# Performance work log

Measured on AMD Instinct MI355X. Metric: run time of the kernel, lower is better.

The kernel has to match this reference:

```python
import jax, jax.numpy as jnp
import numpy as np

T, B, I, H, O = 512, 128, 256, 1024, 256


def setup_inputs() -> dict:
    key = jax.random.key(0)
    ks = jax.random.split(key, 16)
    std = 0.02
    inp = {
        "input_seq": jax.random.normal(ks[0], (T, B, I), dtype=jnp.float32),
        # encoder LSTM (torch gate order i, f, g, o)
        "W_ih_enc": jax.random.normal(ks[1], (4 * H, I), dtype=jnp.float32) * std,
        "W_hh_enc": jax.random.normal(ks[2], (4 * H, H), dtype=jnp.float32) * std,
        "b_ih_enc": jnp.zeros((4 * H,), dtype=jnp.float32),
        "b_hh_enc": jnp.zeros((4 * H,), dtype=jnp.float32),
        # attention: Linear(2H -> H) and score vector v
        "W_attn": jax.random.normal(ks[3], (H, 2 * H), dtype=jnp.float32) * std,
        "b_attn": jnp.zeros((H,), dtype=jnp.float32),
        "v": jax.random.uniform(ks[4], (H,), dtype=jnp.float32),
        # decoder LSTMCell (H -> H)
        "W_ih_dec": jax.random.normal(ks[5], (4 * H, H), dtype=jnp.float32) * std,
        "W_hh_dec": jax.random.normal(ks[6], (4 * H, H), dtype=jnp.float32) * std,
        "b_ih_dec": jnp.zeros((4 * H,), dtype=jnp.float32),
        "b_hh_dec": jnp.zeros((4 * H,), dtype=jnp.float32),
        # decoder linear H -> H
        "W_dec": jax.random.normal(ks[7], (H, H), dtype=jnp.float32) * std,
        "b_dec": jnp.zeros((H,), dtype=jnp.float32),
        # top-level output linear H -> O
        "W_out": jax.random.normal(ks[8], (O, H), dtype=jnp.float32) * std,
        "b_out": jnp.zeros((O,), dtype=jnp.float32),
        "len_out": 30,
    }
    return inp


def _lstm_cell(h, c, x, Wih, Whh, bih, bhh):
    gates = x @ Wih.T + bih + h @ Whh.T + bhh  # [B, 4H]
    i, f, g, o = jnp.split(gates, 4, axis=-1)
    i, f, o = jax.nn.sigmoid(i), jax.nn.sigmoid(f), jax.nn.sigmoid(o)
    c = f * c + i * jnp.tanh(g)
    h = o * jnp.tanh(c)
    return h, c


def reference(input_seq, W_ih_enc, W_hh_enc, b_ih_enc, b_hh_enc,
              W_attn, b_attn, v, W_ih_dec, W_hh_dec, b_ih_dec, b_hh_dec,
              W_dec, b_dec, W_out, b_out, len_out):
    Tdim, Bdim, _ = input_seq.shape
    Hdim = W_hh_enc.shape[1]

    # ---- encoder LSTM over time (seq-first) ----
    h0 = jnp.zeros((Bdim, Hdim), dtype=input_seq.dtype)
    c0 = jnp.zeros((Bdim, Hdim), dtype=input_seq.dtype)

    def enc_step(carry, x_t):
        h, c = carry
        h, c = _lstm_cell(h, c, x_t, W_ih_enc, W_hh_enc, b_ih_enc, b_hh_enc)
        return (h, c), h

    (h_enc, _), context_seq = jax.lax.scan(enc_step, (h0, c0), input_seq)
    # dropout is identity in eval mode

    # ---- precompute context part of Bahdanau energy ----
    # W_attn acts on cat([hidden, context]) => split into hidden / context blocks
    W_h, W_c = W_attn[:, :Hdim], W_attn[:, Hdim:]
    ctx_proj = jnp.einsum('tbh,gh->tbg', context_seq, W_c) + b_attn  # [T,B,H]

    def dec_step(carry, _):
        h, c = carry
        energy = jnp.tanh(h @ W_h.T + ctx_proj)          # [T,B,H]
        scores = jnp.einsum('tbh,h->tb', energy, v)       # [T,B]
        w = jax.nn.softmax(scores, axis=0)                # softmax over time
        context = jnp.einsum('tbh,tb->bh', context_seq, w)  # [B,H]
        h, c = _lstm_cell(h, c, context, W_ih_dec, W_hh_dec, b_ih_dec, b_hh_dec)
        out = jax.nn.relu(h @ W_dec.T + b_dec)
        out = out @ W_out.T + b_out
        return (h, c), out

    _, outputs = jax.lax.scan(dec_step, (h_enc, jnp.zeros_like(h_enc)), None,
                              length=len_out)
    return outputs  # [len_out, B, O]
```

## Files before the change

kernel.cpp:

```cpp
#include <hip/hip_runtime.h>
#include <hip/hip_bf16.h>
#include <type_traits>


static constexpr int T_ = 512, B_ = 128, I_ = 256, H_ = 1024, O_ = 256;

typedef unsigned short ushort;
typedef unsigned long long u64;
typedef __attribute__((ext_vector_type(8))) short bf16x8;
typedef __attribute__((ext_vector_type(4))) float f32x4;
typedef __attribute__((ext_vector_type(8))) _Float16 half8;

__device__ __forceinline__ float bf2f(ushort u) {
    union { unsigned i; float f; } cv; cv.i = ((unsigned)u) << 16; return cv.f;
}
__device__ __forceinline__ ushort f2bf(float f) {
    union { float f; unsigned u; } c; c.f = f;
    unsigned r = c.u + 0x7FFFu + ((c.u >> 16) & 1u);
    return (ushort)(r >> 16);
}
__device__ __forceinline__ float fast_sigmoid(float x) { return 1.f / (1.f + __expf(-x)); }
__device__ __forceinline__ float fast_tanh(float x) {
    float ax = fabsf(x);
    float e = __expf(-2.f * ax);
    float t = (1.f - e) / (1.f + e);
    return copysignf(t, x);
}
__device__ __forceinline__ f32x4 mfma16(bf16x8 a, bf16x8 b, f32x4 c) {
    return __builtin_amdgcn_mfma_f32_16x16x32_bf16(a, b, c, 0, 0, 0);
}
__device__ __forceinline__ bf16x8 ld8(const ushort* p) { return *(const bf16x8*)(const void*)p; }

__device__ __forceinline__ bf16x8 ld8p(const ushort* base, int row, int ko) {
    const size_t t = (size_t)(row >> 7);
    const int b = row & 127;
    const ushort* p0 = base + t * (size_t)(B_ * H_) + ((size_t)((ko >> 2) * B_ + b) << 2);
    union { u64 q[2]; bf16x8 v; } u;
    u.q[0] = *(const u64*)(const void*)p0;
    u.q[1] = *(const u64*)(const void*)(p0 + (B_ << 2));
    return u.v;
}

__device__ __forceinline__ void split8(const float* p, bf16x8& hi, bf16x8& lo) {
    #pragma unroll
    for (int j = 0; j < 8; j++) {
        const float f = p[j];
        const ushort h = f2bf(f);
        hi[j] = (short)h;
        lo[j] = (short)f2bf(f - bf2f(h));
    }
}

__global__ __launch_bounds__(256) void split_w(
    const float* __restrict__ src, int srcld, int coloff,
    ushort* __restrict__ hi, ushort* __restrict__ lo, int K)
{
    const int k = blockIdx.x * 256 + threadIdx.x;
    const int r = blockIdx.y;
    const float f = src[(size_t)r * srcld + coloff + k];
    const ushort h = f2bf(f);
    hi[(size_t)r * K + k] = h;
    lo[(size_t)r * K + k] = f2bf(f - bf2f(h));
}

#define ENC_SMEM_BYTES (32*64*8*2*2 + 8*64*8*2*2 + 16*132*4)
#define LORING_SLOTS 256

__global__ __launch_bounds__(512) void enc_persistent(
    const float* __restrict__ input_seq,
    const ushort* __restrict__ WhhE_h, const ushort* __restrict__ WhhE_l,
    const ushort* __restrict__ WihE_h, const ushort* __restrict__ WihE_l,
    const float* __restrict__ bih, const float* __restrict__ bhh,
    const ushort* __restrict__ hzero,
    ushort* __restrict__ ctx_seq,
    ushort* __restrict__ loring,
    ushort* __restrict__ enc_lo_fin,
    unsigned* __restrict__ bar)
{
    extern __shared__ __align__(16) char smem[];
    ushort* LWh = (ushort*)smem;
    ushort* LWl = LWh + 32 * 64 * 8;
    ushort* LIh = LWl + 32 * 64 * 8;
    ushort* LIl = LIh + 8 * 64 * 8;
    float*  Gt  = (float*)(LIl + 8 * 64 * 8);

    const int tid  = threadIdx.x;
    const int wave = tid >> 6, lane = tid & 63;
    const int quad = lane >> 4, l15 = lane & 15;
    const int bx   = blockIdx.x;
    const int h0   = bx << 2;
    const int wr   = ((l15 >> 2) * H_) + h0 + (l15 & 3);

    {
        const size_t woff = (size_t)wr * H_;
        #pragma unroll
        for (int ii = 0; ii < 4; ii++) {
            const int i   = wave + (ii << 3);
            const int src = (i << 5) + (quad << 3);
            *(bf16x8*)(LWh + ((i << 6) + lane) * 8) = ld8(WhhE_h + woff + src);
            *(bf16x8*)(LWl + ((i << 6) + lane) * 8) = ld8(WhhE_l + woff + src);
        }
        const size_t ioff = (size_t)wr * I_;
        const int src2 = (wave << 5) + (quad << 3);
        *(bf16x8*)(LIh + ((wave << 6) + lane) * 8) = ld8(WihE_h + ioff + src2);
        *(bf16x8*)(LIl + ((wave << 6) + lane) * 8) = ld8(WihE_l + ioff + src2);
    }

    const int bl_  = tid >> 2, hl = tid & 3;
    const int hidx = h0 + hl;
    const float bs0 = bih[hidx]           + bhh[hidx];
    const float bs1 = bih[H_ + hidx]      + bhh[H_ + hidx];
    const float bs2 = bih[2 * H_ + hidx]  + bhh[2 * H_ + hidx];
    const float bs3 = bih[3 * H_ + hidx]  + bhh[3 * H_ + hidx];
    float c_reg = 0.f;
    __syncthreads();

    const int arow = (wave << 4) + l15;
    const size_t xoff = (size_t)arow * I_;

    for (int t = 0; t < T_; t++) {
        const float* xs = input_seq + (size_t)t * (B_ * I_);

        f32x4 acc0 = {0.f, 0.f, 0.f, 0.f}, acc1 = acc0, acc2 = acc0;
        #pragma unroll
        for (int kc = 0; kc < I_; kc += 32) {
            const int i = kc >> 5;
            const bf16x8 bh = *(const bf16x8*)(LIh + ((i << 6) + lane) * 8);
            const bf16x8 bl = *(const bf16x8*)(LIl + ((i << 6) + lane) * 8);
            bf16x8 ah, al;
            split8(xs + xoff + kc + (quad << 3), ah, al);
            acc0 = mfma16(ah, bh, acc0);
            acc1 = mfma16(ah, bl, acc1);
            acc2 = mfma16(al, bh, acc2);
        }

        if (t != 0) {
            if (tid == 0) {
                while (__hip_atomic_load(&bar[1], __ATOMIC_RELAXED,
                                         __HIP_MEMORY_SCOPE_AGENT) < (unsigned)t)
                    __builtin_amdgcn_s_sleep(2);
            }
            __syncthreads();
        }

        const ushort* hi_src = t ? (ctx_seq + (size_t)(t - 1) * (B_ * H_)) : hzero;
        const ushort* lo_src = t ? (loring + (size_t)((t - 1) & (LORING_SLOTS - 1))
                                             * (B_ * H_)) : hzero;
        #pragma unroll 8
        for (int kc = 0; kc < H_; kc += 32) {
            const int i  = kc >> 5;
            const int ko = kc + (quad << 3);
            const bf16x8 bh = *(const bf16x8*)(LWh + ((i << 6) + lane) * 8);
            const bf16x8 bl = *(const bf16x8*)(LWl + ((i << 6) + lane) * 8);
            const bf16x8 ah = ld8p(hi_src, arow, ko);
            const bf16x8 al = ld8p(lo_src, arow, ko);
            acc0 = mfma16(ah, bh, acc0);
            acc1 = mfma16(ah, bl, acc1);
            acc2 = mfma16(al, bh, acc2);
        }
        #pragma unroll
        for (int r = 0; r < 4; r++)
            Gt[l15 * 132 + (wave << 4) + (quad << 2) + r] = acc0[r] + acc1[r] + acc2[r];
        __syncthreads();

        const float gi = Gt[hl * 132 + bl_]        + bs0;
        const float gf = Gt[(4 + hl) * 132 + bl_]  + bs1;
        const float gg = Gt[(8 + hl) * 132 + bl_]  + bs2;
        const float go = Gt[(12 + hl) * 132 + bl_] + bs3;
        const float ig = fast_sigmoid(gi), fg = fast_sigmoid(gf);
        const float gtv = fast_tanh(gg),   og = fast_sigmoid(go);
        c_reg = fg * c_reg + ig * gtv;
        const float hnew = og * fast_tanh(c_reg);
        const ushort hh  = f2bf(hnew);
        const ushort hlo = f2bf(hnew - bf2f(hh));

        const unsigned hp = (unsigned)hh  | (__shfl_down((unsigned)hh, 1)  << 16);
        const unsigned lp = (unsigned)hlo | (__shfl_down((unsigned)hlo, 1) << 16);
        const unsigned pi = ((unsigned)bx << 9) + (unsigned)tid;
        if (!(tid & 1)) {
            __hip_atomic_store((unsigned*)(void*)&ctx_seq[(size_t)t * (B_ * H_) + pi],
                               hp, __ATOMIC_RELAXED, __HIP_MEMORY_SCOPE_AGENT);
            __hip_atomic_store((unsigned*)(void*)
                               &loring[(size_t)(t & (LORING_SLOTS - 1)) * (B_ * H_) + pi],
                               lp, __ATOMIC_RELAXED, __HIP_MEMORY_SCOPE_AGENT);
            if (t == T_ - 1)
                *(unsigned*)(void*)&enc_lo_fin[pi] = lp;
        }

        if (t != T_ - 1) {
            __syncthreads();
            if (tid == 0) {
                const unsigned arrived =
                    __hip_atomic_fetch_add(&bar[0], 1u, __ATOMIC_RELAXED,
                                           __HIP_MEMORY_SCOPE_AGENT) + 1;
                if (arrived == (unsigned)(t + 1) * 256u)
                    __hip_atomic_store(&bar[1], (unsigned)(t + 1),
                                       __ATOMIC_RELAXED, __HIP_MEMORY_SCOPE_AGENT);
            }
        }
    }
}

template<bool WSPLIT, bool XSPLIT, int KX>
__global__ __launch_bounds__(256) void lstm_mfma(
    const ushort* __restrict__ h_hi, const ushort* __restrict__ h_lo,
    const void* __restrict__ x_p, const ushort* __restrict__ x_lo,
    const void* __restrict__ Whh_a, const void* __restrict__ Whh_b,
    const void* __restrict__ Wih_a, const void* __restrict__ Wih_b,
    const float* __restrict__ bih, const float* __restrict__ bhh,
    const float* __restrict__ c_in, float* __restrict__ c_out,
    ushort* __restrict__ h_out_hi, ushort* __restrict__ h_out_lo)
{
    __shared__ float Gt[16][65];
    const int tid = threadIdx.x;
    const int wave = tid >> 6, lane = tid & 63;
    const int quad = lane >> 4, l15 = lane & 15;
    const int h0 = blockIdx.x << 2;
    const int mbase = (blockIdx.y << 6) + (wave << 4);
    const int arow = mbase + l15;
    const int wr = ((l15 >> 2) * H_) + h0 + (l15 & 3);

    f32x4 acc0 = {0.f,0.f,0.f,0.f}, acc1 = acc0, acc2 = acc0;

    {
        const size_t woff = (size_t)wr * H_;
        #pragma unroll 4
        for (int kc = 0; kc < H_; kc += 32) {
            const int ko = kc + quad * 8;
            bf16x8 bh, bl;
            if constexpr (WSPLIT) {
                bh = ld8((const ushort*)Whh_a + woff + ko);
                bl = ld8((const ushort*)Whh_b + woff + ko);
            } else {
                split8((const float*)Whh_a + woff + ko, bh, bl);
            }
            const bf16x8 ah = ld8p(h_hi, arow, ko);
            const bf16x8 al = ld8p(h_lo, arow, ko);
            acc0 = mfma16(ah, bh, acc0);
            acc1 = mfma16(ah, bl, acc1);
            acc2 = mfma16(al, bh, acc2);
        }
    }
    {
        const size_t woff = (size_t)wr * KX;
        #pragma unroll 2
        for (int kc = 0; kc < KX; kc += 32) {
            const int ko = kc + quad * 8;
            bf16x8 bh, bl;
            if constexpr (WSPLIT) {
                bh = ld8((const ushort*)Wih_a + woff + ko);
                bl = ld8((const ushort*)Wih_b + woff + ko);
            } else {
                split8((const float*)Wih_a + woff + ko, bh, bl);
            }
            bf16x8 ah, al;
            if constexpr (XSPLIT) {
                ah = ld8p((const ushort*)x_p, arow, ko);
                al = ld8p(x_lo, arow, ko);
            } else {
                split8((const float*)x_p + (size_t)arow * KX + ko, ah, al);
            }
            acc0 = mfma16(ah, bh, acc0);
            acc1 = mfma16(ah, bl, acc1);
            acc2 = mfma16(al, bh, acc2);
        }
    }
    #pragma unroll
    for (int r = 0; r < 4; r++)
        Gt[l15][(wave << 4) + quad * 4 + r] = acc0[r] + acc1[r] + acc2[r];
    __syncthreads();

    const int bl_ = tid >> 2, hl = tid & 3;
    const int b = (blockIdx.y << 6) + bl_;
    const int hidx = h0 + hl;
    const float gi = Gt[hl][bl_]      + bih[hidx]          + bhh[hidx];
    const float gf = Gt[4 + hl][bl_]  + bih[H_ + hidx]     + bhh[H_ + hidx];
    const float gg = Gt[8 + hl][bl_]  + bih[2 * H_ + hidx] + bhh[2 * H_ + hidx];
    const float go = Gt[12 + hl][bl_] + bih[3 * H_ + hidx] + bhh[3 * H_ + hidx];
    const float ig = fast_sigmoid(gi), fg = fast_sigmoid(gf);
    const float gt = fast_tanh(gg),    og = fast_sigmoid(go);
    const float cold = c_in[b * H_ + hidx];
    const float cnew = fg * cold + ig * gt;
    const float hnew = og * fast_tanh(cnew);
    c_out[b * H_ + hidx] = cnew;
    const ushort hh = f2bf(hnew);
    const size_t op = ((size_t)(hidx >> 2) * B_ + b) * 4 + (hidx & 3);
    h_out_hi[op] = hh;
    h_out_lo[op] = f2bf(hnew - bf2f(hh));
}

template<bool A_LO, int NT, int OM, bool RELU, int K, bool APANEL>
__global__ __launch_bounds__(256) void gemm_mfma(
    const ushort* __restrict__ Ahi, const ushort* __restrict__ Alo, int lda,
    const ushort* __restrict__ Whi, const ushort* __restrict__ Wlo,
    const float* __restrict__ bias,
    void* __restrict__ out0, void* __restrict__ out1, int ldc)
{
    const int tid = threadIdx.x;
    const int wave = tid >> 6, lane = tid & 63;
    const int quad = lane >> 4, l15 = lane & 15;
    const int colbase = (blockIdx.x * NT) << 4;
    const int row = (blockIdx.y << 6) + (wave << 4) + l15;
    const size_t aoff = (size_t)row * lda;

    f32x4 acc0[NT], acc1[NT], acc2[NT];
    #pragma unroll
    for (int nt = 0; nt < NT; nt++) {
        acc0[nt] = {0.f,0.f,0.f,0.f}; acc1[nt] = acc0[nt]; acc2[nt] = acc0[nt];
    }
    size_t woff[NT];
    #pragma unroll
    for (int nt = 0; nt < NT; nt++)
        woff[nt] = (size_t)(colbase + (nt << 4) + l15) * K;

    #pragma unroll 2
    for (int kc = 0; kc < K; kc += 32) {
        const int ko = kc + quad * 8;
        const bf16x8 ah = APANEL ? ld8p(Ahi, row, ko) : ld8(Ahi + aoff + ko);
        bf16x8 al;
        if (A_LO) al = APANEL ? ld8p(Alo, row, ko) : ld8(Alo + aoff + ko);
        #pragma unroll
        for (int nt = 0; nt < NT; nt++) {
            const bf16x8 bh = ld8(Whi + woff[nt] + ko);
            const bf16x8 bl = ld8(Wlo + woff[nt] + ko);
            acc0[nt] = mfma16(ah, bh, acc0[nt]);
            acc1[nt] = mfma16(ah, bl, acc1[nt]);
            if (A_LO) acc2[nt] = mfma16(al, bh, acc2[nt]);
        }
    }
    const size_t orow0 = ((size_t)blockIdx.y << 6) + (wave << 4) + quad * 4;
    const size_t HALF_IDX = (size_t)32768 * 1024;
    #pragma unroll
    for (int nt = 0; nt < NT; nt++) {
        const int col = colbase + (nt << 4) + l15;
        const float bv = bias ? bias[col] : 0.f;
        #pragma unroll
        for (int r = 0; r < 4; r++) {
            float v = acc0[nt][r] + acc1[nt][r] + (A_LO ? acc2[nt][r] : 0.f) + bv;
            if (RELU) v = fmaxf(v, 0.f);
            const size_t idx = (orow0 + r) * (size_t)ldc + col;
            if constexpr (OM == 0) {
                ((float*)out0)[idx] = v;
            } else if constexpr (OM == 3) {
                const size_t idxp = ((size_t)(col >> 2) * B_ + (orow0 + r)) * 4 + (col & 3);
                const ushort h = f2bf(v);
                ((ushort*)out0)[idxp] = h;
                ((ushort*)out1)[idxp] = f2bf(v - bf2f(h));
            } else {
                if (idx < HALF_IDX) ((_Float16*)out0)[idx] = (_Float16)v;
                else                ((_Float16*)out1)[idx - HALF_IDX] = (_Float16)v;
            }
        }
    }
}

__global__ __launch_bounds__(256) void attn_score_kernel(
    const float* __restrict__ q,
    const _Float16* __restrict__ P0, const _Float16* __restrict__ P1,
    const float* __restrict__ v, float* __restrict__ scores)
{
    const int wave = threadIdx.x >> 6, lane = threadIdx.x & 63;
    const int p = (blockIdx.x << 2) + wave;
    const int t = p >> 7, b = p & 127;
    const size_t base = (size_t)(t * B_ + b) * H_ + (lane << 4);
    const size_t HALF_IDX = (size_t)32768 * 1024;
    const _Float16* pp = (base < HALF_IDX) ? (P0 + base) : (P1 + (base - HALF_IDX));

    const half8 u0 = *(const half8*)(const void*)pp;
    const half8 u1 = *(const half8*)(const void*)(pp + 8);
    float pv[16];
    #pragma unroll
    for (int j = 0; j < 8; j++) { pv[j] = (float)u0[j]; pv[8 + j] = (float)u1[j]; }

    const float* qp = q + b * H_ + (lane << 4);
    const float* vp = v + (lane << 4);
    float sum = 0.f;
    #pragma unroll
    for (int j0 = 0; j0 < 16; j0 += 4) {
        const float4 qv = *(const float4*)(qp + j0);
        const float4 vv = *(const float4*)(vp + j0);
        sum += vv.x * fast_tanh(qv.x + pv[j0 + 0]);
        sum += vv.y * fast_tanh(qv.y + pv[j0 + 1]);
        sum += vv.z * fast_tanh(qv.z + pv[j0 + 2]);
        sum += vv.w * fast_tanh(qv.w + pv[j0 + 3]);
    }
    #pragma unroll
    for (int off = 32; off; off >>= 1) sum += __shfl_down(sum, off);
    if (lane == 0) scores[b * T_ + t] = sum;
}

__global__ __launch_bounds__(256) void softmax_kernel(
    const float* __restrict__ scores, float* __restrict__ scT)
{
    __shared__ float red[256];
    const int b = blockIdx.x, tid = threadIdx.x;
    const float s0 = scores[b * T_ + tid];
    const float s1 = scores[b * T_ + tid + 256];
    red[tid] = fmaxf(s0, s1);
    __syncthreads();
    for (int off = 128; off; off >>= 1) {
        if (tid < off) red[tid] = fmaxf(red[tid], red[tid + off]);
        __syncthreads();
    }
    const float mx = red[0];
    __syncthreads();
    const float e0 = __expf(s0 - mx), e1 = __expf(s1 - mx);
    red[tid] = e0 + e1;
    __syncthreads();
    for (int off = 128; off; off >>= 1) {
        if (tid < off) red[tid] += red[tid + off];
        __syncthreads();
    }
    const float inv = 1.f / red[0];
    scT[tid * B_ + b] = e0 * inv;
    scT[(tid + 256) * B_ + b] = e1 * inv;
}

__global__ __launch_bounds__(256) void attn_context_kernel(
    const float* __restrict__ scT, const ushort* __restrict__ ctx,
    ushort* __restrict__ chi, ushort* __restrict__ clo)
{
    const int u = blockIdx.x * 256 + threadIdx.x;
    const int c = u >> 7, b = u & 127;
    const ushort* cp = ctx + ((size_t)(c * B_ + b) << 2);
    const float* wp = scT + b;
    float a0 = 0.f, a1 = 0.f, a2 = 0.f, a3 = 0.f;
    #pragma unroll 4
    for (int t = 0; t < T_; t++) {
        const float w = wp[t << 7];
        const u64 raw = *(const u64*)(const void*)(cp + (size_t)t * (B_ * H_));
        a0 += w * bf2f((ushort)raw);
        a1 += w * bf2f((ushort)(raw >> 16));
        a2 += w * bf2f((ushort)(raw >> 32));
        a3 += w * bf2f((ushort)(raw >> 48));
    }
    const size_t i0 = (size_t)(c * B_ + b) << 2;
    const ushort h0 = f2bf(a0), h1 = f2bf(a1), h2 = f2bf(a2), h3 = f2bf(a3);
    const ushort l0 = f2bf(a0 - bf2f(h0)), l1 = f2bf(a1 - bf2f(h1));
    const ushort l2 = f2bf(a2 - bf2f(h2)), l3 = f2bf(a3 - bf2f(h3));
    *(u64*)(void*)&chi[i0] = (u64)h0 | ((u64)h1 << 16) | ((u64)h2 << 32) | ((u64)h3 << 48);
    *(u64*)(void*)&clo[i0] = (u64)l0 | ((u64)l1 << 16) | ((u64)l2 << 32) | ((u64)l3 << 48);
}

extern "C" void kernel_launch(void* const* d_in, const int* in_sizes, int n_in,
                              void* d_out, int out_size, void* d_ws, size_t ws_size,
                              hipStream_t stream)
{
    const float* input_seq = (const float*)d_in[0];
    const float* W_ih_enc  = (const float*)d_in[1];
    const float* W_hh_enc  = (const float*)d_in[2];
    const float* b_ih_enc  = (const float*)d_in[3];
    const float* b_hh_enc  = (const float*)d_in[4];
    const float* W_attn    = (const float*)d_in[5];
    const float* b_attn    = (const float*)d_in[6];
    const float* v         = (const float*)d_in[7];
    const float* W_ih_dec  = (const float*)d_in[8];
    const float* W_hh_dec  = (const float*)d_in[9];
    const float* b_ih_dec  = (const float*)d_in[10];
    const float* b_hh_dec  = (const float*)d_in[11];
    const float* W_dec     = (const float*)d_in[12];
    const float* b_dec     = (const float*)d_in[13];
    const float* W_out     = (const float*)d_in[14];
    const float* b_out     = (const float*)d_in[15];
    float* out = (float*)d_out;
    const int LEN = out_size / (B_ * O_);
    const int BH = B_ * H_;

    char* ws = (char*)d_ws;
    size_t off = 0;
    auto aus = [&](size_t n) { ushort* p = (ushort*)(ws + off); off += n * 2; return p; };
    auto af  = [&](size_t n) { float*  p = (float*) (ws + off); off += n * 4; return p; };

    ushort* WhhE_h = aus((size_t)4*H_*H_); ushort* WhhE_l = aus((size_t)4*H_*H_);
    ushort* WihE_h = aus((size_t)4*H_*I_); ushort* WihE_l = aus((size_t)4*H_*I_);
    ushort* Wh_h   = aus((size_t)H_*H_);   ushort* Wh_l   = aus((size_t)H_*H_);
    ushort* Wc_h   = aus((size_t)H_*H_);   ushort* Wc_l   = aus((size_t)H_*H_);
    ushort* Wdec_h = aus((size_t)H_*H_);   ushort* Wdec_l = aus((size_t)H_*H_);
    ushort* Wout_h = aus((size_t)O_*H_);   ushort* Wout_l = aus((size_t)O_*H_);

    ushort* ctx_seq = aus((size_t)T_ * BH);
    ushort* hzero   = aus(BH);
    ushort* enc_lo_fin = aus(BH);
    ushort* hd_hi0  = aus(BH); ushort* hd_hi1  = aus(BH);
    ushort* hd_lo0  = aus(BH); ushort* hd_lo1  = aus(BH);
    ushort* ctx_hi  = aus(BH); ushort* ctx_lo  = aus(BH);
    ushort* d1_hi   = aus(BH); ushort* d1_lo   = aus(BH);
    float*  cbuf    = af(BH);
    float*  qbuf    = af(BH);
    float*  scores  = af(B_ * T_);
    float*  scT     = af(B_ * T_);
    unsigned* barbuf = (unsigned*)(ws + off); off += 256;

    ushort* loring = aus((size_t)LORING_SLOTS * BH);
    const size_t P_HALF = (size_t)(T_ / 2) * BH * 2;
    _Float16* P1 = (_Float16*)loring;
    _Float16* P0;
    if (ws_size >= off + P_HALF) {
        P0 = (_Float16*)(ws + off);
    } else {
        P0 = (_Float16*)const_cast<float*>(input_seq);
    }

    auto spl = [&](const float* src, int srcld, int coloff, ushort* hi, ushort* lo,
                   int R, int K) {
        split_w<<<dim3(K / 256, R), 256, 0, stream>>>(src, srcld, coloff, hi, lo, K);
    };
    spl(W_hh_enc, H_,     0,  WhhE_h, WhhE_l, 4 * H_, H_);
    spl(W_ih_enc, I_,     0,  WihE_h, WihE_l, 4 * H_, I_);
    spl(W_attn,   2 * H_, 0,  Wh_h,   Wh_l,   H_,     H_);
    spl(W_attn,   2 * H_, H_, Wc_h,   Wc_l,   H_,     H_);
    spl(W_dec,    H_,     0,  Wdec_h, Wdec_l, H_,     H_);
    spl(W_out,    H_,     0,  Wout_h, Wout_l, O_,     H_);

    hipMemsetAsync(hzero,  0, (size_t)BH * 2, stream);
    hipMemsetAsync(barbuf, 0, 256, stream);

    enc_persistent<<<dim3(H_ / 4), 512, ENC_SMEM_BYTES, stream>>>(
        input_seq, WhhE_h, WhhE_l, WihE_h, WihE_l, b_ih_enc, b_hh_enc,
        hzero, ctx_seq, loring, enc_lo_fin, barbuf);

    gemm_mfma<false, 8, 4, false, H_, true><<<dim3(8, (T_ * B_) / 64), 256, 0, stream>>>(
        ctx_seq, nullptr, H_, Wc_h, Wc_l, b_attn, P0, P1, H_);

    hipMemsetAsync(cbuf, 0, (size_t)BH * 4, stream);
    ushort* dhh[2] = {hd_hi0, hd_hi1};
    ushort* dhl[2] = {hd_lo0, hd_lo1};
    for (int s = 0; s < LEN; s++) {
        const ushort* hi_in = (s == 0) ? ctx_seq + (size_t)(T_ - 1) * BH : dhh[s & 1];
        const ushort* lo_in = (s == 0) ? enc_lo_fin : dhl[s & 1];

        gemm_mfma<true, 1, 0, false, H_, true><<<dim3(H_ / 16, 2), 256, 0, stream>>>(
            hi_in, lo_in, H_, Wh_h, Wh_l, nullptr, qbuf, nullptr, H_);
        attn_score_kernel<<<T_ * B_ / 4, 256, 0, stream>>>(qbuf, P0, P1, v, scores);
        softmax_kernel<<<B_, 256, 0, stream>>>(scores, scT);
        attn_context_kernel<<<BH / 4 / 256, 256, 0, stream>>>(scT, ctx_seq, ctx_hi, ctx_lo);
        lstm_mfma<false, true, H_><<<dim3(H_ / 4, 2), 256, 0, stream>>>(
            hi_in, lo_in, (const void*)ctx_hi, ctx_lo,
            W_hh_dec, nullptr, W_ih_dec, nullptr, b_ih_dec, b_hh_dec,
            cbuf, cbuf, dhh[(s + 1) & 1], dhl[(s + 1) & 1]);
        gemm_mfma<true, 1, 3, true, H_, true><<<dim3(H_ / 16, 2), 256, 0, stream>>>(
            dhh[(s + 1) & 1], dhl[(s + 1) & 1], H_, Wdec_h, Wdec_l, b_dec,
            d1_hi, d1_lo, H_);
        gemm_mfma<true, 1, 0, false, H_, true><<<dim3(O_ / 16, 2), 256, 0, stream>>>(
            d1_hi, d1_lo, H_, Wout_h, Wout_l, b_out,
            out + (size_t)s * B_ * O_, nullptr, O_);
    }
    (void)in_sizes; (void)n_in;
}
```

Baseline: 16.64 ms.

## Use two-level tree barrier in encoder and pre-pack inputs into bf16 hi/lo pairs

The encoder's grid-wide step barrier changes from a single global counter hit by all 256 blocks to a two-level tree. Sixteen padded leaf counters each gather sixteen blocks, and a root counter publishes the step flag. This is meant to cut atomic contention and barrier latency on each of the 512 serial timesteps. Separately, a new pack_x kernel converts input_seq in place into packed bf16 hi/lo words, so the encoder loads the pairs directly instead of splitting fp32 on every step. The in-place overwrite of the caller's input buffer is a risk: a repeated call on the same buffer would re-pack already packed data.

Result: no change. 16.71 ms (+0.4%).

```diff
diff --git a/kernel.cpp b/kernel.cpp
--- a/kernel.cpp
+++ b/kernel.cpp
@@ -9,6 +9,7 @@
 typedef unsigned long long u64;
 typedef __attribute__((ext_vector_type(8))) short bf16x8;
 typedef __attribute__((ext_vector_type(4))) float f32x4;
+typedef __attribute__((ext_vector_type(4))) unsigned uint4_t;
 typedef __attribute__((ext_vector_type(8))) _Float16 half8;
 
 __device__ __forceinline__ float bf2f(ushort u) {
@@ -63,11 +64,28 @@
     lo[(size_t)r * K + k] = f2bf(f - bf2f(h));
 }
 
+__global__ __launch_bounds__(256) void pack_x(float* __restrict__ x)
+{
+    const size_t i = ((size_t)blockIdx.x * 256 + threadIdx.x) * 8;
+    float4 a = *(const float4*)(x + i);
+    float4 b = *(const float4*)(x + i + 4);
+    unsigned w[8];
+    const float f_[8] = {a.x, a.y, a.z, a.w, b.x, b.y, b.z, b.w};
+    #pragma unroll
+    for (int j = 0; j < 8; j++) {
+        const ushort h = f2bf(f_[j]);
+        const ushort l = f2bf(f_[j] - bf2f(h));
+        w[j] = (unsigned)h | ((unsigned)l << 16);
+    }
+    *(uint4_t*)(void*)(x + i)     = uint4_t{w[0], w[1], w[2], w[3]};
+    *(uint4_t*)(void*)(x + i + 4) = uint4_t{w[4], w[5], w[6], w[7]};
+}
+
 #define ENC_SMEM_BYTES (32*64*8*2*2 + 8*64*8*2*2 + 16*132*4)
 #define LORING_SLOTS 256
 
 __global__ __launch_bounds__(512) void enc_persistent(
-    const float* __restrict__ input_seq,
+    const unsigned* __restrict__ xpk,
     const ushort* __restrict__ WhhE_h, const ushort* __restrict__ WhhE_l,
     const ushort* __restrict__ WihE_h, const ushort* __restrict__ WihE_l,
     const float* __restrict__ bih, const float* __restrict__ bhh,
@@ -119,7 +137,7 @@
     const size_t xoff = (size_t)arow * I_;
 
     for (int t = 0; t < T_; t++) {
-        const float* xs = input_seq + (size_t)t * (B_ * I_);
+        const unsigned* xs = xpk + (size_t)t * (B_ * I_) + xoff;
 
         f32x4 acc0 = {0.f, 0.f, 0.f, 0.f}, acc1 = acc0, acc2 = acc0;
         #pragma unroll
@@ -127,8 +145,17 @@
             const int i = kc >> 5;
             const bf16x8 bh = *(const bf16x8*)(LIh + ((i << 6) + lane) * 8);
             const bf16x8 bl = *(const bf16x8*)(LIl + ((i << 6) + lane) * 8);
+            const uint4_t w0 = *(const uint4_t*)(const void*)(xs + kc + (quad << 3));
+            const uint4_t w1 = *(const uint4_t*)(const void*)(xs + kc + (quad << 3) + 4);
             bf16x8 ah, al;
-            split8(xs + xoff + kc + (quad << 3), ah, al);
+            ah[0] = (short)(w0.x & 0xffff); al[0] = (short)(w0.x >> 16);
+            ah[1] = (short)(w0.y & 0xffff); al[1] = (short)(w0.y >> 16);
+            ah[2] = (short)(w0.z & 0xffff); al[2] = (short)(w0.z >> 16);
+            ah[3] = (short)(w0.w & 0xffff); al[3] = (short)(w0.w >> 16);
+            ah[4] = (short)(w1.x & 0xffff); al[4] = (short)(w1.x >> 16);
+            ah[5] = (short)(w1.y & 0xffff); al[5] = (short)(w1.y >> 16);
+            ah[6] = (short)(w1.z & 0xffff); al[6] = (short)(w1.z >> 16);
+            ah[7] = (short)(w1.w & 0xffff); al[7] = (short)(w1.w >> 16);
             acc0 = mfma16(ah, bh, acc0);
             acc1 = mfma16(ah, bl, acc1);
             acc2 = mfma16(al, bh, acc2);
@@ -136,7 +163,7 @@
 
         if (t != 0) {
             if (tid == 0) {
-                while (__hip_atomic_load(&bar[1], __ATOMIC_RELAXED,
+                while (__hip_atomic_load(&bar[0], __ATOMIC_RELAXED,
                                          __HIP_MEMORY_SCOPE_AGENT) < (unsigned)t)
                     __builtin_amdgcn_s_sleep(2);
             }
@@ -190,12 +217,17 @@
         if (t != T_ - 1) {
             __syncthreads();
             if (tid == 0) {
-                const unsigned arrived =
-                    __hip_atomic_fetch_add(&bar[0], 1u, __ATOMIC_RELAXED,
-                                           __HIP_MEMORY_SCOPE_AGENT) + 1;
-                if (arrived == (unsigned)(t + 1) * 256u)
-                    __hip_atomic_store(&bar[1], (unsigned)(t + 1),
-                                       __ATOMIC_RELAXED, __HIP_MEMORY_SCOPE_AGENT);
+                const unsigned tgt = (unsigned)(t + 1) * 16u;
+                unsigned* leaf = bar + 64 + ((bx & 15) << 4);
+                const unsigned la = __hip_atomic_fetch_add(leaf, 1u, __ATOMIC_RELAXED,
+                                                           __HIP_MEMORY_SCOPE_AGENT) + 1;
+                if (la == tgt) {
+                    const unsigned ra = __hip_atomic_fetch_add(&bar[32], 1u,
+                                            __ATOMIC_RELAXED, __HIP_MEMORY_SCOPE_AGENT) + 1;
+                    if (ra == tgt)
+                        __hip_atomic_store(&bar[0], (unsigned)(t + 1),
+                                           __ATOMIC_RELAXED, __HIP_MEMORY_SCOPE_AGENT);
+                }
             }
         }
     }
@@ -489,7 +521,7 @@
     float*  qbuf    = af(BH);
     float*  scores  = af(B_ * T_);
     float*  scT     = af(B_ * T_);
-    unsigned* barbuf = (unsigned*)(ws + off); off += 256;
+    unsigned* barbuf = (unsigned*)(ws + off); off += 4096;
 
     ushort* loring = aus((size_t)LORING_SLOTS * BH);
     const size_t P_HALF = (size_t)(T_ / 2) * BH * 2;
@@ -512,12 +544,15 @@
     spl(W_dec,    H_,     0,  Wdec_h, Wdec_l, H_,     H_);
     spl(W_out,    H_,     0,  Wout_h, Wout_l, O_,     H_);
 
+    pack_x<<<(T_ * B_ * I_) / (256 * 8), 256, 0, stream>>>(
+        const_cast<float*>(input_seq));
+
     hipMemsetAsync(hzero,  0, (size_t)BH * 2, stream);
-    hipMemsetAsync(barbuf, 0, 256, stream);
+    hipMemsetAsync(barbuf, 0, 4096, stream);
 
     enc_persistent<<<dim3(H_ / 4), 512, ENC_SMEM_BYTES, stream>>>(
-        input_seq, WhhE_h, WhhE_l, WihE_h, WihE_l, b_ih_enc, b_hh_enc,
-        hzero, ctx_seq, loring, enc_lo_fin, barbuf);
+        (const unsigned*)input_seq, WhhE_h, WhhE_l, WihE_h, WihE_l,
+        b_ih_enc, b_hh_enc, hzero, ctx_seq, loring, enc_lo_fin, barbuf);
 
     gemm_mfma<false, 8, 4, false, H_, true><<<dim3(8, (T_ * B_) / 64), 256, 0, stream>>>(
         ctx_seq, nullptr, H_, Wc_h, Wc_l, b_attn, P0, P1, H_);
```
